# Performance work log

Hardware: AMD Instinct MI355X
Metric: run time of the kernel (lower is better)

Reference implementation:

```python
import jax, jax.numpy as jnp
import numpy as np
import math
jax.config.update("jax_enable_x64", True)

BITS = 10

def _morton3d(coords):
    # coords: [B,N,3] floats in [0,1]; replicates torch morton3D exactly (int64 bit interleave)
    max_val = 2 ** BITS - 1
    def quant(c):
        return jnp.clip((c * max_val).astype(jnp.int64), 0, max_val)
    xv, yv, zv = quant(coords[..., 0]), quant(coords[..., 1]), quant(coords[..., 2])
    def interleave(v):
        v = v & 2097151
        v = v | (v << 32)
        v = v & 8725724278095871
        v = v | ((v << 16) & 8725728556220671)
        v = v | ((v << 8) & 282506020581391)
        v = v | ((v << 4) & 294878547030211)
        v = v | ((v << 2) & 321685687669321)
        return v
    return interleave(xv) | (interleave(yv) << 1) | (interleave(zv) << 2)


def setup_inputs() -> dict:
    key = jax.random.key(0)
    ks = jax.random.split(key, 8)
    B, N, D, BN = 16, 8192, 256, 32
    R = max(1, BN // 8)  # = 4
    x = jax.random.normal(ks[0], (B, N, D), dtype=jnp.float32)
    coords = jax.random.uniform(ks[1], (B, N, 3), dtype=jnp.float32)
    s_d = 1.0 / math.sqrt(D + 1)
    s_b = 1.0 / math.sqrt(BN)
    Wd = jax.random.normal(ks[2], (BN, D + 1), dtype=jnp.float32) * s_d
    bd = jax.random.normal(ks[3], (BN,), dtype=jnp.float32) * s_d
    U = jax.random.normal(ks[4], (BN, R), dtype=jnp.float32) * 0.1
    V = jax.random.normal(ks[5], (BN, R), dtype=jnp.float32) * 0.1
    logit_d = jnp.ones((BN,), dtype=jnp.float32) * 4.0
    Wu = jax.random.normal(ks[6], (D, BN), dtype=jnp.float32) * s_b
    bu = jax.random.normal(ks[7], (D,), dtype=jnp.float32) * s_b
    return {"x": x, "coords": coords, "Wd": Wd, "bd": bd, "U": U, "V": V,
            "logit_d": logit_d, "Wu": Wu, "bu": bu}


def reference(x, coords, Wd, bd, U, V, logit_d, Wu, bu):
    B, N, D = x.shape
    # morton-order permutation of points
    order = jnp.argsort(_morton3d(coords), axis=-1)          # [B,N] int
    x_perm = jnp.take_along_axis(x, order[..., None], axis=1)  # [B,N,D]
    # NOTE: original concatenates the UNPERMUTED radius (faithful to source)
    r = jnp.linalg.norm(coords, axis=-1, keepdims=True)      # [B,N,1]
    z = jnp.concatenate([x_perm, r], axis=-1)                # [B,N,D+1]
    z = jax.nn.relu(jnp.einsum('bnd,kd->bnk', z, Wd) + bd)   # [B,N,BN]
    # spectral filter along the point axis
    Zf = jnp.fft.fft(z, axis=1)                              # complex64 [B,N,BN]
    w = jnp.linspace(0.0, 2.0 * math.pi, N, dtype=jnp.float32)
    d = jnp.clip(logit_d, -10.0, 10.0)
    H = jnp.exp(-w[:, None] * d[None, :])                    # [N,BN]
    y = jnp.fft.ifft(Zf * H[None], axis=1).real.astype(jnp.float32)
    mix = U @ V.T                                            # [BN,BN] low-rank
    z = y @ mix                                              # [B,N,BN]
    out = jnp.einsum('bnk,dk->bnd', z, Wu) + bu              # [B,N,D]
    return x + out  # dropout = identity (eval mode)
```

## Files before the change

kernel.cpp:

```cpp
#include <hip/hip_runtime.h>
#include <math.h>

#define B_    16
#define N_    8192
#define D_    256
#define BN_   32
#define R_    4
#define LOGN  13

typedef float  f32x4  __attribute__((ext_vector_type(4)));
typedef short  s16x8  __attribute__((ext_vector_type(8)));
typedef unsigned long long ull;
typedef ull    ull2   __attribute__((ext_vector_type(2)));

__device__ __forceinline__ int PAD(int i) { return i + (i >> 4); }

__device__ __forceinline__ ull interleave3(ull v) {
    v = v & 2097151ULL;
    v = v | (v << 32);
    v = v & 8725724278095871ULL;
    v = v | ((v << 16) & 8725728556220671ULL);
    v = v | ((v << 8)  & 282506020581391ULL);
    v = v | ((v << 4)  & 294878547030211ULL);
    v = v | ((v << 2)  & 321685687669321ULL);
    return v;
}

__device__ __forceinline__ long long quant10(float c) {
    long long v = (long long)(c * 1023.0f);
    v = v < 0 ? 0 : (v > 1023 ? 1023 : v);
    return v;
}

__device__ __forceinline__ unsigned short f2bf(float f) {
    unsigned u = __float_as_uint(f);
    u = (u + 0x7FFF + ((u >> 16) & 1)) >> 16;
    return (unsigned short)u;
}

__device__ __forceinline__ unsigned cvtpk_bf16(float lo, float hi) {
    unsigned r;
    asm("v_cvt_pk_bf16_f32 %0, %1, %2" : "=v"(r) : "v"(lo), "v"(hi));
    return r;
}

__device__ __forceinline__ void cswap(ull& a, ull& b, bool up) {
    ull lo = a < b ? a : b;
    ull hi = a < b ? b : a;
    a = up ? lo : hi;
    b = up ? hi : lo;
}

__global__ __launch_bounds__(1024)
void fat_kernel(const float* __restrict__ x,
                const float* __restrict__ coords,
                const float* __restrict__ Wd,
                int* __restrict__ order,
                float* __restrict__ z_pk) {
    extern __shared__ ull skey[];
    const int bid = blockIdx.x;
    const int t   = threadIdx.x;

    if (bid < B_) {
        const int b = bid;
        {
            const int i0 = t * 8;
            ull K[8];
            #pragma unroll
            for (int j = 0; j < 8; ++j) {
                const float* c = coords + ((size_t)b * N_ + i0 + j) * 3;
                ull mx = interleave3((ull)quant10(c[0]));
                ull my = interleave3((ull)quant10(c[1]));
                ull mz = interleave3((ull)quant10(c[2]));
                ull m = mx | (my << 1) | (mz << 2);
                K[j] = (m << LOGN) | (ull)(i0 + j);
            }
            cswap(K[0], K[1], true);  cswap(K[2], K[3], false);
            cswap(K[4], K[5], true);  cswap(K[6], K[7], false);
            cswap(K[0], K[2], true);  cswap(K[1], K[3], true);
            cswap(K[4], K[6], false); cswap(K[5], K[7], false);
            cswap(K[0], K[1], true);  cswap(K[2], K[3], true);
            cswap(K[4], K[5], false); cswap(K[6], K[7], false);
            const bool U = ((t & 1) == 0);
            cswap(K[0], K[4], U); cswap(K[1], K[5], U);
            cswap(K[2], K[6], U); cswap(K[3], K[7], U);
            cswap(K[0], K[2], U); cswap(K[1], K[3], U);
            cswap(K[4], K[6], U); cswap(K[5], K[7], U);
            cswap(K[0], K[1], U); cswap(K[2], K[3], U);
            cswap(K[4], K[5], U); cswap(K[6], K[7], U);
            ull2* p2 = (ull2*)&skey[i0];
            #pragma unroll
            for (int j = 0; j < 4; ++j) { ull2 w; w.x = K[2*j]; w.y = K[2*j+1]; p2[j] = w; }
        }
        __syncthreads();

        for (int k = 4; k <= LOGN; ++k) {
            const int size = 1 << k;
            int s = size >> 1;

            while (s >= 32) {
                const int q  = s >> 2;
                const int jj = t & (q - 1);
                const int i0 = ((t - jj) << 3) + jj;
                ull K[8];
                #pragma unroll
                for (int j = 0; j < 8; ++j) K[j] = skey[i0 + j * q];
                const bool up = ((i0 & size) == 0);
                cswap(K[0], K[4], up); cswap(K[1], K[5], up);
                cswap(K[2], K[6], up); cswap(K[3], K[7], up);
                cswap(K[0], K[2], up); cswap(K[1], K[3], up);
                cswap(K[4], K[6], up); cswap(K[5], K[7], up);
                cswap(K[0], K[1], up); cswap(K[2], K[3], up);
                cswap(K[4], K[5], up); cswap(K[6], K[7], up);
                #pragma unroll
                for (int j = 0; j < 8; ++j) skey[i0 + j * q] = K[j];
                __syncthreads();
                s >>= 3;
            }

            if (s == 16) {
                #pragma unroll
                for (int u = 0; u < 2; ++u) {
                    const int p  = t + u * 1024;
                    const int jj = p & 7;
                    const int i0 = ((p - jj) << 2) + jj;
                    ull K0 = skey[i0], K1 = skey[i0 + 8];
                    ull K2 = skey[i0 + 16], K3 = skey[i0 + 24];
                    const bool up = ((i0 & size) == 0);
                    cswap(K0, K2, up); cswap(K1, K3, up);
                    cswap(K0, K1, up); cswap(K2, K3, up);
                    skey[i0] = K0; skey[i0 + 8] = K1;
                    skey[i0 + 16] = K2; skey[i0 + 24] = K3;
                }
                __syncthreads();
            } else if (s == 8) {
                #pragma unroll
                for (int u = 0; u < 4; ++u) {
                    const int p  = t + u * 1024;
                    const int jj = p & 7;
                    const int i  = ((p - jj) << 1) + jj;
                    ull a = skey[i], c = skey[i + 8];
                    cswap(a, c, ((i & size) == 0));
                    skey[i] = a; skey[i + 8] = c;
                }
                __syncthreads();
            }

            {
                const int i0 = t * 8;
                ull K[8];
                ull2* p2 = (ull2*)&skey[i0];
                #pragma unroll
                for (int j = 0; j < 4; ++j) { ull2 w = p2[j]; K[2*j] = w.x; K[2*j+1] = w.y; }
                const bool up = ((i0 & size) == 0);
                cswap(K[0], K[4], up); cswap(K[1], K[5], up);
                cswap(K[2], K[6], up); cswap(K[3], K[7], up);
                cswap(K[0], K[2], up); cswap(K[1], K[3], up);
                cswap(K[4], K[6], up); cswap(K[5], K[7], up);
                cswap(K[0], K[1], up); cswap(K[2], K[3], up);
                cswap(K[4], K[5], up); cswap(K[6], K[7], up);
                if (k == LOGN) {
                    #pragma unroll
                    for (int j = 0; j < 8; ++j)
                        order[b * N_ + i0 + j] = (int)(K[j] & (ull)(N_ - 1));
                } else {
                    #pragma unroll
                    for (int j = 0; j < 4; ++j) { ull2 w; w.x = K[2*j]; w.y = K[2*j+1]; p2[j] = w; }
                    __syncthreads();
                }
            }
        }
    } else {
        const int zb  = bid - B_;
        const int b   = zb >> 5;
        const int m0  = (zb & 31) << 8;
        const int w   = t >> 6;
        const int l   = t & 63;
        const int lg  = l >> 4;
        const int lm  = l & 15;
        char* wlds = (char*)skey;

        {
            const int i0  = t * 8;
            const int row = i0 >> 8;
            const int col = i0 & 255;
            const float* src = Wd + (size_t)row * 257 + col;
            unsigned off = ((unsigned)row << 9) + ((unsigned)col << 1);
            off ^= (unsigned)(row & 7) << 4;
            ushort4 p0, p1;
            p0.x = f2bf(src[0]); p0.y = f2bf(src[1]);
            p0.z = f2bf(src[2]); p0.w = f2bf(src[3]);
            p1.x = f2bf(src[4]); p1.y = f2bf(src[5]);
            p1.z = f2bf(src[6]); p1.w = f2bf(src[7]);
            *(ushort4*)(wlds + off)     = p0;
            *(ushort4*)(wlds + off + 8) = p1;
        }
        __syncthreads();

        s16x8 wf0[8], wf1[8];
        #pragma unroll
        for (int kc = 0; kc < 8; ++kc) {
            const unsigned doff = (unsigned)(kc * 64 + lg * 16);
            const unsigned sw   = (unsigned)(lm & 7) << 4;
            wf0[kc] = *(const s16x8*)(wlds + ((((unsigned)lm << 9) + doff) ^ sw));
            wf1[kc] = *(const s16x8*)(wlds + ((((unsigned)(16 + lm) << 9) + doff) ^ sw));
        }

        const int xr = w * 16 + lm;
        const float* xrow = x + ((size_t)(b * N_ + m0 + xr)) * D_;

        f32x4 acc0 = {0.f, 0.f, 0.f, 0.f};
        f32x4 acc1 = {0.f, 0.f, 0.f, 0.f};
        #pragma unroll
        for (int kc = 0; kc < 8; ++kc) {
            const float4 va = *(const float4*)(xrow + kc * 32 + lg * 8);
            const float4 vb = *(const float4*)(xrow + kc * 32 + lg * 8 + 4);
            union { s16x8 v; unsigned u[4]; } bu_;
            bu_.u[0] = cvtpk_bf16(va.x, va.y);
            bu_.u[1] = cvtpk_bf16(va.z, va.w);
            bu_.u[2] = cvtpk_bf16(vb.x, vb.y);
            bu_.u[3] = cvtpk_bf16(vb.z, vb.w);
            acc0 = __builtin_amdgcn_mfma_f32_16x16x32_bf16(wf0[kc], bu_.v, acc0, 0, 0, 0);
            acc1 = __builtin_amdgcn_mfma_f32_16x16x32_bf16(wf1[kc], bu_.v, acc1, 0, 0, 0);
        }

        const int m = m0 + xr;
        float* zb_ = z_pk + ((size_t)(b * N_ + m)) * BN_;
        float4 v0, v1;
        v0.x = acc0[0]; v0.y = acc0[1]; v0.z = acc0[2]; v0.w = acc0[3];
        v1.x = acc1[0]; v1.y = acc1[1]; v1.z = acc1[2]; v1.w = acc1[3];
        *(float4*)(zb_ + lg * 4)      = v0;
        *(float4*)(zb_ + 16 + lg * 4) = v1;
    }
}

__global__ __launch_bounds__(512)
void zgather_kernel(const float* __restrict__ z_pk,
                    const float* __restrict__ coords,
                    const float* __restrict__ Wd,
                    const float* __restrict__ bd,
                    const int*   __restrict__ order,
                    const float* __restrict__ Wu,
                    const float* __restrict__ V,
                    float*       __restrict__ G,
                    float*       __restrict__ z_kp) {
    __shared__ float ltile[64][33];
    __shared__ float sWdLast[BN_];
    __shared__ float sbd[BN_];
    const int blk = blockIdx.x;
    const int b   = blk >> 7;
    const int p0  = (blk & 127) << 6;
    const int t   = threadIdx.x;

    if (blk < 8 && t < 128) {
        const int dl = blk * 32 + (t >> 2);
        const int r  = t & 3;
        float s = 0.0f;
        #pragma unroll
        for (int kk = 0; kk < BN_; ++kk) s += Wu[dl * BN_ + kk] * V[kk * R_ + r];
        G[dl * R_ + r] = s;
    }

    if (t < BN_) { sWdLast[t] = Wd[(size_t)t * 257 + 256]; sbd[t] = bd[t]; }
    __syncthreads();

    {
        const int sl = t >> 3;
        const int kc = t & 7;
        const int p  = p0 + sl;
        const int od = order[b * N_ + p];
        float4 v = *(const float4*)(z_pk + ((size_t)(b * N_ + od)) * BN_ + kc * 4);
        const float* c = coords + ((size_t)(b * N_ + p)) * 3;
        const float rr = sqrtf(c[0] * c[0] + c[1] * c[1] + c[2] * c[2]);
        v.x = fmaxf(v.x + rr * sWdLast[kc * 4 + 0] + sbd[kc * 4 + 0], 0.0f);
        v.y = fmaxf(v.y + rr * sWdLast[kc * 4 + 1] + sbd[kc * 4 + 1], 0.0f);
        v.z = fmaxf(v.z + rr * sWdLast[kc * 4 + 2] + sbd[kc * 4 + 2], 0.0f);
        v.w = fmaxf(v.w + rr * sWdLast[kc * 4 + 3] + sbd[kc * 4 + 3], 0.0f);
        ltile[sl][kc * 4 + 0] = v.x;
        ltile[sl][kc * 4 + 1] = v.y;
        ltile[sl][kc * 4 + 2] = v.z;
        ltile[sl][kc * 4 + 3] = v.w;
    }
    __syncthreads();

    {
        const int k  = t >> 4;
        const int pc = t & 15;
        float4 o;
        o.x = ltile[pc * 4 + 0][k];
        o.y = ltile[pc * 4 + 1][k];
        o.z = ltile[pc * 4 + 2][k];
        o.w = ltile[pc * 4 + 3][k];
        *(float4*)(z_kp + (size_t)(b * BN_ + k) * N_ + p0 + pc * 4) = o;
    }
}

__device__ __forceinline__ float2 cmul(float2 a, float2 b) {
    return make_float2(a.x * b.x - a.y * b.y, a.x * b.y + a.y * b.x);
}
__device__ __forceinline__ float2 sdmix(float S, float D, float2 P, float2 Q) {
    return make_float2(S * P.x + D * Q.x, S * P.y - D * Q.y);
}

__global__ __launch_bounds__(512)
void fft_filter_kernel(float* __restrict__ zy,
                       const float* __restrict__ logit_d) {
    extern __shared__ float2 cbuf[];

    const int bk = blockIdx.x;
    const int b  = bk >> 4;
    const int kp = bk & 15;
    const int t  = threadIdx.x;

    float* row1 = zy + (size_t)(b * BN_ + 2 * kp) * N_;
    float* row2 = row1 + N_;

    float d1 = fminf(fmaxf(logit_d[2 * kp],     -10.0f), 10.0f);
    float d2 = fminf(fmaxf(logit_d[2 * kp + 1], -10.0f), 10.0f);

    const float cpi  = 3.14159265358979323846f;
    const float c2pi = 6.28318530717958647692f;
    const float A    = c2pi * 8192.0f / 8191.0f;

    const float Eh1 = __expf(-0.5f * A * d1), E1 = Eh1 * Eh1;
    const float Eh2 = __expf(-0.5f * A * d2), E2 = Eh2 * Eh2;

    {
        const int h = 4096, hh = 2048;
        #pragma unroll
        for (int u = 0; u < 4; ++u) {
            const int i0 = t + u * 512;
            float2 c0 = make_float2(row1[i0],            row2[i0]);
            float2 c1 = make_float2(row1[i0 + hh],       row2[i0 + hh]);
            float2 c2 = make_float2(row1[i0 + h],        row2[i0 + h]);
            float2 c3 = make_float2(row1[i0 + h + hh],   row2[i0 + h + hh]);
            float sA, cA;
            __sincosf(-cpi * (float)i0 / (float)h, &sA, &cA);
            const float2 twA1 = make_float2(cA, sA);
            const float2 twA2 = make_float2(sA, -cA);
            const float2 twB  = make_float2(2.0f * cA * cA - 1.0f, 2.0f * sA * cA);
            float2 a0 = make_float2(c0.x + c2.x, c0.y + c2.y);
            float2 a1 = make_float2(c1.x + c3.x, c1.y + c3.y);
            float2 b0 = cmul(make_float2(c0.x - c2.x, c0.y - c2.y), twA1);
            float2 b1 = cmul(make_float2(c1.x - c3.x, c1.y - c3.y), twA2);
            cbuf[PAD(i0)]          = make_float2(a0.x + a1.x, a0.y + a1.y);
            cbuf[PAD(i0 + hh)]     = cmul(make_float2(a0.x - a1.x, a0.y - a1.y), twB);
            cbuf[PAD(i0 + h)]      = make_float2(b0.x + b1.x, b0.y + b1.y);
            cbuf[PAD(i0 + h + hh)] = cmul(make_float2(b0.x - b1.x, b0.y - b1.y), twB);
        }
        __syncthreads();
    }

    #pragma unroll
    for (int h = 1024; h >= 4; h >>= 2) {
        const int hh = h >> 1;
        #pragma unroll
        for (int u = 0; u < 4; ++u) {
            const int q   = t + u * 512;
            const int jj  = q & (hh - 1);
            const int i0  = ((q - jj) << 2) + jj;
            float2 c0 = cbuf[PAD(i0)];
            float2 c1 = cbuf[PAD(i0 + hh)];
            float2 c2 = cbuf[PAD(i0 + h)];
            float2 c3 = cbuf[PAD(i0 + h + hh)];
            float sA, cA;
            __sincosf(-cpi * (float)jj / (float)h, &sA, &cA);
            const float2 twA1 = make_float2(cA, sA);
            const float2 twA2 = make_float2(sA, -cA);
            const float2 twB  = make_float2(2.0f * cA * cA - 1.0f, 2.0f * sA * cA);
            float2 a0 = make_float2(c0.x + c2.x, c0.y + c2.y);
            float2 a1 = make_float2(c1.x + c3.x, c1.y + c3.y);
            float2 b0 = cmul(make_float2(c0.x - c2.x, c0.y - c2.y), twA1);
            float2 b1 = cmul(make_float2(c1.x - c3.x, c1.y - c3.y), twA2);
            cbuf[PAD(i0)]          = make_float2(a0.x + a1.x, a0.y + a1.y);
            cbuf[PAD(i0 + hh)]     = cmul(make_float2(a0.x - a1.x, a0.y - a1.y), twB);
            cbuf[PAD(i0 + h)]      = make_float2(b0.x + b1.x, b0.y + b1.y);
            cbuf[PAD(i0 + h + hh)] = cmul(make_float2(b0.x - b1.x, b0.y - b1.y), twB);
        }
        __syncthreads();
    }

    {
        #pragma unroll
        for (int v = 0; v < 4; ++v) {
            const int u = t + v * 512;
            if (u == 0) {
                {
                    float2 g0 = cbuf[0], g1 = cbuf[1];
                    float2 Pa = make_float2(g0.x + g1.x, g0.y + g1.y);
                    float2 Pb = make_float2(g0.x - g1.x, g0.y - g1.y);
                    float2 Ra = Pa;
                    float Sb = 0.5f * (Eh1 + Eh2), Db = 0.5f * (Eh1 - Eh2);
                    float2 Rb = sdmix(Sb, Db, Pb, Pb);
                    cbuf[0] = make_float2(Ra.x + Rb.x, Ra.y + Rb.y);
                    cbuf[1] = make_float2(Ra.x - Rb.x, Ra.y - Rb.y);
                }
                {
                    float wu = c2pi * 2048.0f / 8191.0f;
                    float h1 = __expf(-wu * d1), h2 = __expf(-wu * d2);
                    float h1b = h1 * Eh1, h2b = h2 * Eh2;
                    float Hs1a = 0.5f * (h1 + E1 / h1);
                    float Hs2a = 0.5f * (h2 + E2 / h2);
                    float Hs1b = 0.5f * (h1b + E1 / h1b);
                    float Hs2b = 0.5f * (h2b + E2 / h2b);
                    float Sa = 0.5f * (Hs1a + Hs2a), Da = 0.5f * (Hs1a - Hs2a);
                    float Sb = 0.5f * (Hs1b + Hs2b), Db = 0.5f * (Hs1b - Hs2b);
                    float2 g0 = cbuf[2], g1 = cbuf[3];
                    float2 Pa = make_float2(g0.x + g1.x, g0.y + g1.y);
                    float2 Pb = make_float2(g0.x - g1.x, g0.y - g1.y);
                    float2 Ra = sdmix(Sa, Da, Pa, Pb);
                    float2 Rb = sdmix(Sb, Db, Pb, Pa);
                    cbuf[2] = make_float2(Ra.x + Rb.x, Ra.y + Rb.y);
                    cbuf[3] = make_float2(Ra.x - Rb.x, Ra.y - Rb.y);
                }
            } else {
                const int u2 = 4096 - u;
                const int c  = (int)(__brev((unsigned)u)  >> 20);
                const int c2 = (int)(__brev((unsigned)u2) >> 20);
                const int s0 = PAD(2 * c),  s1 = PAD(2 * c + 1);
                const int s2 = PAD(2 * c2), s3 = PAD(2 * c2 + 1);
                float2 g0 = cbuf[s0], g1 = cbuf[s1];
                float2 q0 = cbuf[s2], q1 = cbuf[s3];
                float2 Pa  = make_float2(g0.x + g1.x, g0.y + g1.y);
                float2 Pb  = make_float2(g0.x - g1.x, g0.y - g1.y);
                float2 Pa2 = make_float2(q0.x + q1.x, q0.y + q1.y);
                float2 Pb2 = make_float2(q0.x - q1.x, q0.y - q1.y);
                float wu = c2pi * (float)u / 8191.0f;
                float h1 = __expf(-wu * d1), h2 = __expf(-wu * d2);
                float h1b = h1 * Eh1, h2b = h2 * Eh2;
                float Hs1a = 0.5f * (h1 + E1 / h1);
                float Hs2a = 0.5f * (h2 + E2 / h2);
                float Hs1b = 0.5f * (h1b + E1 / h1b);
                float Hs2b = 0.5f * (h2b + E2 / h2b);
                float Sa = 0.5f * (Hs1a + Hs2a), Da = 0.5f * (Hs1a - Hs2a);
                float Sb = 0.5f * (Hs1b + Hs2b), Db = 0.5f * (Hs1b - Hs2b);
                float2 Ra  = sdmix(Sa, Da, Pa,  Pb2);
                float2 Rb2 = sdmix(Sa, Da, Pb2, Pa);
                float2 Rb  = sdmix(Sb, Db, Pb,  Pa2);
                float2 Ra2 = sdmix(Sb, Db, Pa2, Pb);
                cbuf[s0] = make_float2(Ra.x + Rb.x,   Ra.y + Rb.y);
                cbuf[s1] = make_float2(Ra.x - Rb.x,   Ra.y - Rb.y);
                cbuf[s2] = make_float2(Ra2.x + Rb2.x, Ra2.y + Rb2.y);
                cbuf[s3] = make_float2(Ra2.x - Rb2.x, Ra2.y - Rb2.y);
            }
        }
        __syncthreads();
    }

    #pragma unroll
    for (int h = 2; h <= 512; h <<= 2) {
        #pragma unroll
        for (int u = 0; u < 4; ++u) {
            const int q  = t + u * 512;
            const int jj = q & (h - 1);
            const int i0 = ((q - jj) << 2) + jj;
            float2 c0 = cbuf[PAD(i0)];
            float2 c1 = cbuf[PAD(i0 + h)];
            float2 c2 = cbuf[PAD(i0 + 2 * h)];
            float2 c3 = cbuf[PAD(i0 + 3 * h)];
            float sa, ca;
            __sincosf(cpi * (float)jj / (float)(2 * h), &sa, &ca);
            const float2 tw1  = make_float2(2.0f * ca * ca - 1.0f, 2.0f * sa * ca);
            const float2 tw2a = make_float2(ca, sa);
            const float2 tw2b = make_float2(-sa, ca);
            float2 t0 = cmul(c1, tw1);
            float2 a0 = make_float2(c0.x + t0.x, c0.y + t0.y);
            float2 a1 = make_float2(c0.x - t0.x, c0.y - t0.y);
            float2 t1 = cmul(c3, tw1);
            float2 b0 = make_float2(c2.x + t1.x, c2.y + t1.y);
            float2 b1 = make_float2(c2.x - t1.x, c2.y - t1.y);
            float2 t2 = cmul(b0, tw2a);
            cbuf[PAD(i0)]         = make_float2(a0.x + t2.x, a0.y + t2.y);
            cbuf[PAD(i0 + 2 * h)] = make_float2(a0.x - t2.x, a0.y - t2.y);
            float2 t3 = cmul(b1, tw2b);
            cbuf[PAD(i0 + h)]     = make_float2(a1.x + t3.x, a1.y + t3.y);
            cbuf[PAD(i0 + 3 * h)] = make_float2(a1.x - t3.x, a1.y - t3.y);
        }
        __syncthreads();
    }

    {
        const int h = 2048;
        const float inv = 1.0f / (float)N_;
        #pragma unroll
        for (int u = 0; u < 4; ++u) {
            const int jj = t + u * 512;
            const int i0 = jj;
            float2 c0 = cbuf[PAD(i0)];
            float2 c1 = cbuf[PAD(i0 + h)];
            float2 c2 = cbuf[PAD(i0 + 2 * h)];
            float2 c3 = cbuf[PAD(i0 + 3 * h)];
            float sa, ca;
            __sincosf(cpi * (float)jj / (float)(2 * h), &sa, &ca);
            const float2 tw1  = make_float2(2.0f * ca * ca - 1.0f, 2.0f * sa * ca);
            const float2 tw2a = make_float2(ca, sa);
            const float2 tw2b = make_float2(-sa, ca);
            float2 t0 = cmul(c1, tw1);
            float2 a0 = make_float2(c0.x + t0.x, c0.y + t0.y);
            float2 a1 = make_float2(c0.x - t0.x, c0.y - t0.y);
            float2 t1 = cmul(c3, tw1);
            float2 b0 = make_float2(c2.x + t1.x, c2.y + t1.y);
            float2 b1 = make_float2(c2.x - t1.x, c2.y - t1.y);
            float2 t2 = cmul(b0, tw2a);
            float2 o0 = make_float2(a0.x + t2.x, a0.y + t2.y);
            float2 o2 = make_float2(a0.x - t2.x, a0.y - t2.y);
            float2 t3 = cmul(b1, tw2b);
            float2 o1 = make_float2(a1.x + t3.x, a1.y + t3.y);
            float2 o3 = make_float2(a1.x - t3.x, a1.y - t3.y);
            row1[i0]         = o0.x * inv;  row2[i0]         = o0.y * inv;
            row1[i0 + h]     = o1.x * inv;  row2[i0 + h]     = o1.y * inv;
            row1[i0 + 2*h]   = o2.x * inv;  row2[i0 + 2*h]   = o2.y * inv;
            row1[i0 + 3*h]   = o3.x * inv;  row2[i0 + 3*h]   = o3.y * inv;
        }
    }
}

__global__ __launch_bounds__(256)
void out_kernel(const float* __restrict__ x,
                const float* __restrict__ y_t,
                const float* __restrict__ U,
                const float* __restrict__ G,
                const float* __restrict__ bu,
                float*       __restrict__ out) {
    __shared__ float ttile[64][R_ + 1];
    const int blk = blockIdx.x;
    const int b   = blk >> 7;
    const int n0  = (blk & 127) << 6;
    const int t   = threadIdx.x;

    {
        const int r = t >> 6, nl = t & 63;
        const float* yb = y_t + (size_t)b * BN_ * N_ + n0 + nl;
        float s = 0.0f;
        #pragma unroll
        for (int kk = 0; kk < BN_; ++kk) s += yb[(size_t)kk * N_] * U[kk * R_ + r];
        ttile[nl][r] = s;
    }
    __syncthreads();

    const int d4 = t & 63, rg = t >> 6;
    const float4 g0 = *(const float4*)(G + (d4 * 4 + 0) * 4);
    const float4 g1 = *(const float4*)(G + (d4 * 4 + 1) * 4);
    const float4 g2 = *(const float4*)(G + (d4 * 4 + 2) * 4);
    const float4 g3 = *(const float4*)(G + (d4 * 4 + 3) * 4);
    const float4 bv = *(const float4*)(bu + d4 * 4);
    const float4* xb = (const float4*)(x   + ((size_t)(b * N_ + n0)) * D_);
    float4*       ob = (float4*)      (out + ((size_t)(b * N_ + n0)) * D_);
    #pragma unroll 4
    for (int nl = rg; nl < 64; nl += 4) {
        const float t0 = ttile[nl][0], t1 = ttile[nl][1];
        const float t2 = ttile[nl][2], t3 = ttile[nl][3];
        const float4 xv = xb[nl * 64 + d4];
        float4 o;
        o.x = xv.x + t0 * g0.x + t1 * g0.y + t2 * g0.z + t3 * g0.w + bv.x;
        o.y = xv.y + t0 * g1.x + t1 * g1.y + t2 * g1.z + t3 * g1.w + bv.y;
        o.z = xv.z + t0 * g2.x + t1 * g2.y + t2 * g2.z + t3 * g2.w + bv.z;
        o.w = xv.w + t0 * g3.x + t1 * g3.y + t2 * g3.z + t3 * g3.w + bv.w;
        ob[nl * 64 + d4] = o;
    }
}

extern "C" void kernel_launch(void* const* d_in, const int* in_sizes, int n_in,
                              void* d_out, int out_size, void* d_ws, size_t ws_size,
                              hipStream_t stream) {
    const float* x       = (const float*)d_in[0];
    const float* coords  = (const float*)d_in[1];
    const float* Wd      = (const float*)d_in[2];
    const float* bd      = (const float*)d_in[3];
    const float* U       = (const float*)d_in[4];
    const float* V       = (const float*)d_in[5];
    const float* logit_d = (const float*)d_in[6];
    const float* Wu      = (const float*)d_in[7];
    const float* bu      = (const float*)d_in[8];
    float* out = (float*)d_out;

    char* ws = (char*)d_ws;
    int*   order = (int*)ws;
    float* G     = (float*)(ws + 1536 * 1024);
    float* zpk   = (float*)(ws + 2048 * 1024);
    float* zkp   = (float*)(ws + (2048 + 16384) * 1024);

    fat_kernel   <<<dim3(B_ + 512),    dim3(1024), 64 * 1024, stream>>>(x, coords, Wd, order, zpk);
    zgather_kernel<<<dim3(B_ * 128),   dim3(512),  0, stream>>>(zpk, coords, Wd, bd, order, Wu, V, G, zkp);
    fft_filter_kernel<<<dim3(B_ * 16), dim3(512),  8704 * 8, stream>>>(zkp, logit_d);
    out_kernel   <<<dim3(B_ * 128),    dim3(256),  0, stream>>>(x, zkp, U, G, bu, out);
}
```

Measured before the change: 135.0 us.

## Split Morton bitonic sort into two half-sorts plus a merge kernel

The per-batch 8192-key bitonic sort, previously one 1024-thread block per batch, now runs as two 512-thread blocks per batch that each sort 4096 keys in opposite directions and write raw keys to workspace. A new sort2_kernel does the final merge stage and emits the order indices. The projection blocks in the fused kernel also shrink to 512 threads and 128 rows, with twice as many blocks. The aim is more parallelism and less LDS per block for the critical-path sort, at the cost of an extra kernel launch and a global round-trip of the keys.

Result: faster. 118.4 us (-12.3%).

```diff
diff --git a/kernel.cpp b/kernel.cpp
--- a/kernel.cpp
+++ b/kernel.cpp
@@ -51,29 +51,33 @@
     b = up ? hi : lo;
 }
 
-__global__ __launch_bounds__(1024)
+__global__ __launch_bounds__(512)
 void fat_kernel(const float* __restrict__ x,
                 const float* __restrict__ coords,
                 const float* __restrict__ Wd,
-                int* __restrict__ order,
+                ull* __restrict__ keys,
                 float* __restrict__ z_pk) {
     extern __shared__ ull skey[];
     const int bid = blockIdx.x;
     const int t   = threadIdx.x;
 
-    if (bid < B_) {
-        const int b = bid;
+    if (bid < 2 * B_) {
+        const int b = bid >> 1;
+        const int h = bid & 1;
+        const int gbase = h * 4096;
+
         {
             const int i0 = t * 8;
             ull K[8];
             #pragma unroll
             for (int j = 0; j < 8; ++j) {
-                const float* c = coords + ((size_t)b * N_ + i0 + j) * 3;
+                const int gi = gbase + i0 + j;
+                const float* c = coords + ((size_t)b * N_ + gi) * 3;
                 ull mx = interleave3((ull)quant10(c[0]));
                 ull my = interleave3((ull)quant10(c[1]));
                 ull mz = interleave3((ull)quant10(c[2]));
                 ull m = mx | (my << 1) | (mz << 2);
-                K[j] = (m << LOGN) | (ull)(i0 + j);
+                K[j] = (m << LOGN) | (ull)gi;
             }
             cswap(K[0], K[1], true);  cswap(K[2], K[3], false);
             cswap(K[4], K[5], true);  cswap(K[6], K[7], false);
@@ -94,7 +98,7 @@
         }
         __syncthreads();
 
-        for (int k = 4; k <= LOGN; ++k) {
+        for (int k = 4; k <= 12; ++k) {
             const int size = 1 << k;
             int s = size >> 1;
 
@@ -105,7 +109,7 @@
                 ull K[8];
                 #pragma unroll
                 for (int j = 0; j < 8; ++j) K[j] = skey[i0 + j * q];
-                const bool up = ((i0 & size) == 0);
+                const bool up = (((gbase + i0) & size) == 0);
                 cswap(K[0], K[4], up); cswap(K[1], K[5], up);
                 cswap(K[2], K[6], up); cswap(K[3], K[7], up);
                 cswap(K[0], K[2], up); cswap(K[1], K[3], up);
@@ -121,12 +125,12 @@
             if (s == 16) {
                 #pragma unroll
                 for (int u = 0; u < 2; ++u) {
-                    const int p  = t + u * 1024;
+                    const int p  = t + u * 512;
                     const int jj = p & 7;
                     const int i0 = ((p - jj) << 2) + jj;
                     ull K0 = skey[i0], K1 = skey[i0 + 8];
                     ull K2 = skey[i0 + 16], K3 = skey[i0 + 24];
-                    const bool up = ((i0 & size) == 0);
+                    const bool up = (((gbase + i0) & size) == 0);
                     cswap(K0, K2, up); cswap(K1, K3, up);
                     cswap(K0, K1, up); cswap(K2, K3, up);
                     skey[i0] = K0; skey[i0 + 8] = K1;
@@ -136,11 +140,11 @@
             } else if (s == 8) {
                 #pragma unroll
                 for (int u = 0; u < 4; ++u) {
-                    const int p  = t + u * 1024;
+                    const int p  = t + u * 512;
                     const int jj = p & 7;
                     const int i  = ((p - jj) << 1) + jj;
                     ull a = skey[i], c = skey[i + 8];
-                    cswap(a, c, ((i & size) == 0));
+                    cswap(a, c, (((gbase + i) & size) == 0));
                     skey[i] = a; skey[i + 8] = c;
                 }
                 __syncthreads();
@@ -152,17 +156,17 @@
                 ull2* p2 = (ull2*)&skey[i0];
                 #pragma unroll
                 for (int j = 0; j < 4; ++j) { ull2 w = p2[j]; K[2*j] = w.x; K[2*j+1] = w.y; }
-                const bool up = ((i0 & size) == 0);
+                const bool up = (((gbase + i0) & size) == 0);
                 cswap(K[0], K[4], up); cswap(K[1], K[5], up);
                 cswap(K[2], K[6], up); cswap(K[3], K[7], up);
                 cswap(K[0], K[2], up); cswap(K[1], K[3], up);
                 cswap(K[4], K[6], up); cswap(K[5], K[7], up);
                 cswap(K[0], K[1], up); cswap(K[2], K[3], up);
                 cswap(K[4], K[5], up); cswap(K[6], K[7], up);
-                if (k == LOGN) {
+                if (k == 12) {
                     #pragma unroll
                     for (int j = 0; j < 8; ++j)
-                        order[b * N_ + i0 + j] = (int)(K[j] & (ull)(N_ - 1));
+                        keys[(size_t)b * N_ + gbase + i0 + j] = K[j];
                 } else {
                     #pragma unroll
                     for (int j = 0; j < 4; ++j) { ull2 w; w.x = K[2*j]; w.y = K[2*j+1]; p2[j] = w; }
@@ -171,9 +175,9 @@
             }
         }
     } else {
-        const int zb  = bid - B_;
-        const int b   = zb >> 5;
-        const int m0  = (zb & 31) << 8;
+        const int zb  = bid - 2 * B_;
+        const int b   = zb >> 6;
+        const int m0  = (zb & 63) << 7;
         const int w   = t >> 6;
         const int l   = t & 63;
         const int lg  = l >> 4;
@@ -181,19 +185,27 @@
         char* wlds = (char*)skey;
 
         {
-            const int i0  = t * 8;
+            const int i0  = t * 16;
             const int row = i0 >> 8;
             const int col = i0 & 255;
             const float* src = Wd + (size_t)row * 257 + col;
-            unsigned off = ((unsigned)row << 9) + ((unsigned)col << 1);
-            off ^= (unsigned)(row & 7) << 4;
-            ushort4 p0, p1;
-            p0.x = f2bf(src[0]); p0.y = f2bf(src[1]);
-            p0.z = f2bf(src[2]); p0.w = f2bf(src[3]);
-            p1.x = f2bf(src[4]); p1.y = f2bf(src[5]);
-            p1.z = f2bf(src[6]); p1.w = f2bf(src[7]);
-            *(ushort4*)(wlds + off)     = p0;
-            *(ushort4*)(wlds + off + 8) = p1;
+            const unsigned sw   = (unsigned)(row & 7) << 4;
+            const unsigned base = ((unsigned)row << 9) + ((unsigned)col << 1);
+            ushort4 a0, a1, b0, b1;
+            a0.x = f2bf(src[0]);  a0.y = f2bf(src[1]);
+            a0.z = f2bf(src[2]);  a0.w = f2bf(src[3]);
+            a1.x = f2bf(src[4]);  a1.y = f2bf(src[5]);
+            a1.z = f2bf(src[6]);  a1.w = f2bf(src[7]);
+            b0.x = f2bf(src[8]);  b0.y = f2bf(src[9]);
+            b0.z = f2bf(src[10]); b0.w = f2bf(src[11]);
+            b1.x = f2bf(src[12]); b1.y = f2bf(src[13]);
+            b1.z = f2bf(src[14]); b1.w = f2bf(src[15]);
+            const unsigned o0 = base ^ sw;
+            const unsigned o1 = (base + 16) ^ sw;
+            *(ushort4*)(wlds + o0)     = a0;
+            *(ushort4*)(wlds + o0 + 8) = a1;
+            *(ushort4*)(wlds + o1)     = b0;
+            *(ushort4*)(wlds + o1 + 8) = b1;
         }
         __syncthreads();
 
@@ -201,9 +213,9 @@
         #pragma unroll
         for (int kc = 0; kc < 8; ++kc) {
             const unsigned doff = (unsigned)(kc * 64 + lg * 16);
-            const unsigned sw   = (unsigned)(lm & 7) << 4;
-            wf0[kc] = *(const s16x8*)(wlds + ((((unsigned)lm << 9) + doff) ^ sw));
-            wf1[kc] = *(const s16x8*)(wlds + ((((unsigned)(16 + lm) << 9) + doff) ^ sw));
+            const unsigned swA  = (unsigned)(lm & 7) << 4;
+            wf0[kc] = *(const s16x8*)(wlds + ((((unsigned)lm << 9) + doff) ^ swA));
+            wf1[kc] = *(const s16x8*)(wlds + ((((unsigned)(16 + lm) << 9) + doff) ^ swA));
         }
 
         const int xr = w * 16 + lm;
@@ -231,6 +243,59 @@
         v1.x = acc1[0]; v1.y = acc1[1]; v1.z = acc1[2]; v1.w = acc1[3];
         *(float4*)(zb_ + lg * 4)      = v0;
         *(float4*)(zb_ + 16 + lg * 4) = v1;
+    }
+}
+
+__global__ __launch_bounds__(512)
+void sort2_kernel(const ull* __restrict__ keys, int* __restrict__ order) {
+    __shared__ ull skey[4096];
+    const int b = blockIdx.x >> 1;
+    const int h = blockIdx.x & 1;
+    const int t = threadIdx.x;
+    const int gbase = h * 4096;
+
+    for (int i = t; i < 4096; i += 512) {
+        ull a = keys[(size_t)b * N_ + i];
+        ull c = keys[(size_t)b * N_ + 4096 + i];
+        ull lo = a < c ? a : c;
+        ull hi = a < c ? c : a;
+        skey[i] = h == 0 ? lo : hi;
+    }
+    __syncthreads();
+
+    #pragma unroll
+    for (int q = 512; q >= 8; q >>= 3) {
+        const int jj = t & (q - 1);
+        const int i0 = ((t - jj) << 3) + jj;
+        ull K[8];
+        #pragma unroll
+        for (int j = 0; j < 8; ++j) K[j] = skey[i0 + j * q];
+        cswap(K[0], K[4], true); cswap(K[1], K[5], true);
+        cswap(K[2], K[6], true); cswap(K[3], K[7], true);
+        cswap(K[0], K[2], true); cswap(K[1], K[3], true);
+        cswap(K[4], K[6], true); cswap(K[5], K[7], true);
+        cswap(K[0], K[1], true); cswap(K[2], K[3], true);
+        cswap(K[4], K[5], true); cswap(K[6], K[7], true);
+        #pragma unroll
+        for (int j = 0; j < 8; ++j) skey[i0 + j * q] = K[j];
+        __syncthreads();
+    }
+
+    {
+        const int i0 = t * 8;
+        ull K[8];
+        ull2* p2 = (ull2*)&skey[i0];
+        #pragma unroll
+        for (int j = 0; j < 4; ++j) { ull2 w = p2[j]; K[2*j] = w.x; K[2*j+1] = w.y; }
+        cswap(K[0], K[4], true); cswap(K[1], K[5], true);
+        cswap(K[2], K[6], true); cswap(K[3], K[7], true);
+        cswap(K[0], K[2], true); cswap(K[1], K[3], true);
+        cswap(K[4], K[6], true); cswap(K[5], K[7], true);
+        cswap(K[0], K[1], true); cswap(K[2], K[3], true);
+        cswap(K[4], K[5], true); cswap(K[6], K[7], true);
+        #pragma unroll
+        for (int j = 0; j < 8; ++j)
+            order[b * N_ + gbase + i0 + j] = (int)(K[j] & (ull)(N_ - 1));
     }
 }
 
@@ -576,12 +641,14 @@
 
     char* ws = (char*)d_ws;
     int*   order = (int*)ws;
+    ull*   keys  = (ull*)(ws + 512 * 1024);
     float* G     = (float*)(ws + 1536 * 1024);
     float* zpk   = (float*)(ws + 2048 * 1024);
     float* zkp   = (float*)(ws + (2048 + 16384) * 1024);
 
-    fat_kernel   <<<dim3(B_ + 512),    dim3(1024), 64 * 1024, stream>>>(x, coords, Wd, order, zpk);
-    zgather_kernel<<<dim3(B_ * 128),   dim3(512),  0, stream>>>(zpk, coords, Wd, bd, order, Wu, V, G, zkp);
-    fft_filter_kernel<<<dim3(B_ * 16), dim3(512),  8704 * 8, stream>>>(zkp, logit_d);
-    out_kernel   <<<dim3(B_ * 128),    dim3(256),  0, stream>>>(x, zkp, U, G, bu, out);
-}
+    fat_kernel   <<<dim3(2 * B_ + 1024), dim3(512), 32 * 1024, stream>>>(x, coords, Wd, keys, zpk);
+    sort2_kernel <<<dim3(2 * B_),        dim3(512), 0, stream>>>(keys, order);
+    zgather_kernel<<<dim3(B_ * 128),     dim3(512), 0, stream>>>(zpk, coords, Wd, bd, order, Wu, V, G, zkp);
+    fft_filter_kernel<<<dim3(B_ * 16),   dim3(512), 8704 * 8, stream>>>(zkp, logit_d);
+    out_kernel   <<<dim3(B_ * 128),      dim3(256), 0, stream>>>(x, zkp, U, G, bu, out);
+}
```
